# Performance work log

Measured on AMD Instinct MI355X. Metric: run time of the kernel, lower is better.

Reference implementation:

```python
import jax, jax.numpy as jnp
import numpy as np

DIM = 512
HEADS = 8
DIM_HEAD = DIM // 8          # 64
M_LAND = DIM // 2            # 256 landmarks
PINV_ITERS = 6
KS = 33                      # residual depthwise conv kernel
EPS = 1e-8
LN_EPS = 1e-5


def setup_inputs() -> dict:
    key = jax.random.key(0)
    ks = jax.random.split(key, 5)
    b, n = 2, 8192
    inner = HEADS * DIM_HEAD
    x = jax.random.normal(ks[0], (b, n, DIM), jnp.float32)
    mask = jnp.ones((b, n), jnp.bool_)
    w_qkv = jax.random.normal(ks[1], (DIM, 3 * inner), jnp.float32) / np.sqrt(DIM)
    w_out = jax.random.normal(ks[2], (inner, DIM), jnp.float32) / np.sqrt(inner)
    b_out = jnp.zeros((DIM,), jnp.float32)
    conv_w = jax.random.normal(ks[3], (HEADS, 1, KS, 1), jnp.float32) / np.sqrt(KS)
    ln_w = jnp.ones((DIM,), jnp.float32)
    ln_b = jnp.zeros((DIM,), jnp.float32)
    return dict(x=x, mask=mask, ln_w=ln_w, ln_b=ln_b,
                w_qkv=w_qkv, w_out=w_out, b_out=b_out, conv_w=conv_w)


def _moore_penrose_pinv(x, iters):
    # lucidrains iterative pinv: z0 = x^T / (max(col_sums) * max(row_sums))
    abs_x = jnp.abs(x)
    col = abs_x.sum(-1)
    row = abs_x.sum(-2)
    z = jnp.swapaxes(x, -1, -2) / (jnp.max(col) * jnp.max(row))
    I = jnp.eye(x.shape[-1], dtype=x.dtype)
    for _ in range(iters):
        xz = x @ z
        z = 0.25 * z @ (13 * I - xz @ (15 * I - xz @ (7 * I - xz)))
    return z


def reference(x, mask, ln_w, ln_b, w_qkv, w_out, b_out, conv_w):
    b, n, _ = x.shape
    # LayerNorm (pre-norm)
    mu = x.mean(-1, keepdims=True)
    var = ((x - mu) ** 2).mean(-1, keepdims=True)
    xn = (x - mu) / jnp.sqrt(var + LN_EPS) * ln_w + ln_b
    # front-pad seq to multiple of num_landmarks (static; no-op when divisible)
    pad = (M_LAND - n % M_LAND) % M_LAND
    if pad:
        xn = jnp.pad(xn, ((0, 0), (pad, 0), (0, 0)))
        mask = jnp.pad(mask, ((0, 0), (pad, 0)), constant_values=False)
    N = n + pad
    qkv = xn @ w_qkv
    q, k, v = jnp.split(qkv, 3, axis=-1)
    rs = lambda t: t.reshape(b, N, HEADS, DIM_HEAD).transpose(0, 2, 1, 3)  # b h N d
    q, k, v = rs(q), rs(k), rs(v)
    m3 = mask[:, None, :]                       # b 1 N
    mf = m3[..., None].astype(q.dtype)
    q, k, v = q * mf, k * mf, v * mf
    q = q * (DIM_HEAD ** -0.5)
    l = N // M_LAND                             # tokens per landmark
    ql = q.reshape(b, HEADS, M_LAND, l, DIM_HEAD).sum(3)
    kl = k.reshape(b, HEADS, M_LAND, l, DIM_HEAD).sum(3)
    m_land_sum = m3.astype(q.dtype).reshape(b, 1, M_LAND, l).sum(-1)   # b 1 M
    divisor = m_land_sum[..., None] + EPS
    ql = ql / divisor
    kl = kl / divisor
    m_land = m_land_sum > 0                     # b 1 M
    sim1 = jnp.einsum('bhid,bhjd->bhij', q, kl)    # b h N M
    sim2 = jnp.einsum('bhid,bhjd->bhij', ql, kl)   # b h M M
    sim3 = jnp.einsum('bhid,bhjd->bhij', ql, k)    # b h M N
    NEG = -jnp.finfo(q.dtype).max
    sim1 = jnp.where(m3[..., None] & m_land[..., None, :], sim1, NEG)
    sim2 = jnp.where(m_land[..., None] & m_land[..., None, :], sim2, NEG)
    sim3 = jnp.where(m_land[..., None] & m3[..., None, :], sim3, NEG)
    a1 = jax.nn.softmax(sim1, -1)
    a2 = jax.nn.softmax(sim2, -1)
    a3 = jax.nn.softmax(sim3, -1)
    a2_inv = _moore_penrose_pinv(a2, PINV_ITERS)
    out = (a1 @ a2_inv) @ (a3 @ v)              # b h N d
    # residual depthwise conv over sequence dim (per head)
    res = jax.lax.conv_general_dilated(
        v, conv_w, window_strides=(1, 1),
        padding=((KS // 2, KS // 2), (0, 0)),
        dimension_numbers=('NCHW', 'OIHW', 'NCHW'),
        feature_group_count=HEADS)
    out = out + res
    out = out.transpose(0, 2, 1, 3).reshape(b, N, HEADS * DIM_HEAD)
    out = out @ w_out + b_out                   # dropout is identity at eval
    out = out[:, -n:]
    return x + out
```

## Files before the change

kernel.cpp:

```cpp
#include <hip/hip_runtime.h>


typedef __attribute__((ext_vector_type(8))) short bf16x8;
typedef __attribute__((ext_vector_type(4))) float f32x4;

static __device__ __forceinline__ ushort f2bf(float f) {
  union { float f; unsigned u; } c; c.f = f;
  const unsigned r = c.u + 0x7fffu + ((c.u >> 16) & 1u);
  return (ushort)(r >> 16);
}
static __device__ __forceinline__ float bf2f(ushort u) {
  union { unsigned u; float f; } c; c.u = ((unsigned)u) << 16;
  return c.f;
}

typedef __attribute__((address_space(1))) const unsigned int guint;
typedef __attribute__((address_space(3))) unsigned int luint;
static __device__ __forceinline__ void gload_lds16(const void* g, void* l) {
  __builtin_amdgcn_global_load_lds((guint*)g, (luint*)l, 16, 0, 0);
}

__global__ __launch_bounds__(256) void ln_kernel(const float* __restrict__ x,
                                                 const float* __restrict__ w,
                                                 const float* __restrict__ b,
                                                 ushort* __restrict__ xn) {
  const int row = blockIdx.x;
  const int t = threadIdx.x;
  const float* xr = x + (long long)row * 512;
  float v0 = xr[t], v1 = xr[t + 256];
  __shared__ float red[8];
  float s = v0 + v1;
#pragma unroll
  for (int o = 32; o; o >>= 1) s += __shfl_xor(s, o);
  if ((t & 63) == 0) red[t >> 6] = s;
  __syncthreads();
  const float mu = (red[0] + red[1] + red[2] + red[3]) * (1.0f / 512.0f);
  const float d0 = v0 - mu, d1 = v1 - mu;
  float qs = d0 * d0 + d1 * d1;
#pragma unroll
  for (int o = 32; o; o >>= 1) qs += __shfl_xor(qs, o);
  if ((t & 63) == 0) red[4 + (t >> 6)] = qs;
  __syncthreads();
  const float var = (red[4] + red[5] + red[6] + red[7]) * (1.0f / 512.0f);
  const float rs = rsqrtf(var + 1e-5f);
  ushort* xo = xn + (long long)row * 512;
  xo[t] = f2bf(d0 * rs * w[t] + b[t]);
  xo[t + 256] = f2bf(d1 * rs * w[t + 256] + b[t + 256]);
}

__global__ __launch_bounds__(256) void convert_T_bf16(const float* __restrict__ in,
                                                      ushort* __restrict__ out,
                                                      int R, int Cc) {
  const long long i = (long long)blockIdx.x * 256 + threadIdx.x;
  if (i >= (long long)R * Cc) return;
  const int c = (int)(i / R), r = (int)(i % R);
  out[i] = f2bf(in[(long long)r * Cc + c]);
}

__global__ __launch_bounds__(256) void gemm_bf16(
    const ushort* __restrict__ A, const ushort* __restrict__ Bt,
    float* __restrict__ C, ushort* __restrict__ uq, ushort* __restrict__ uk,
    ushort* __restrict__ uv,
    const float* __restrict__ bias, const float* __restrict__ xres,
    int K, int mode) {
  const int tid = threadIdx.x;
  const int wave = tid >> 6, lane = tid & 63;
  const int quad = lane >> 4, l16 = lane & 15;

  const int gx = gridDim.x;
  const int nwg = gx * gridDim.y;
  const int hid = blockIdx.y * gx + blockIdx.x;
  const int wid = (hid & 7) * (nwg >> 3) + (hid >> 3);
  const int tm = (wid / gx) * 128, tn = (wid % gx) * 128;

  const int wr = (wave >> 1) * 64, wc = (wave & 1) * 64;
  __shared__ __align__(16) ushort As[128 * 32];
  __shared__ __align__(16) ushort Bs[128 * 32];

  f32x4 acc[4][4];
#pragma unroll
  for (int i = 0; i < 4; ++i)
#pragma unroll
    for (int j = 0; j < 4; ++j) acc[i][j] = (f32x4)0.f;

  const int r0 = tid >> 2;
  const int c0 = (tid & 3) * 8;
  const ushort* gA0 = A + (long long)(tm + r0) * K + c0;
  const ushort* gA1 = A + (long long)(tm + 64 + r0) * K + c0;
  const ushort* gB0 = Bt + (long long)(tn + r0) * K + c0;
  const ushort* gB1 = Bt + (long long)(tn + 64 + r0) * K + c0;
  ushort* lA0 = As + (wave * 64) * 8;
  ushort* lA1 = As + (256 + wave * 64) * 8;
  ushort* lB0 = Bs + (wave * 64) * 8;
  ushort* lB1 = Bs + (256 + wave * 64) * 8;

  for (int kb = 0; kb < K; kb += 32) {
    __syncthreads();
    gload_lds16(gA0 + kb, lA0);
    gload_lds16(gA1 + kb, lA1);
    gload_lds16(gB0 + kb, lB0);
    gload_lds16(gB1 + kb, lB1);
    __syncthreads();
    bf16x8 af[4], bfr[4];
#pragma unroll
    for (int t = 0; t < 4; ++t) {
      af[t] = *(const bf16x8*)&As[(wr + t * 16 + l16) * 32 + quad * 8];
      bfr[t] = *(const bf16x8*)&Bs[(wc + t * 16 + l16) * 32 + quad * 8];
    }
#pragma unroll
    for (int i = 0; i < 4; ++i)
#pragma unroll
      for (int j = 0; j < 4; ++j)
        acc[i][j] = __builtin_amdgcn_mfma_f32_16x16x32_bf16(af[i], bfr[j], acc[i][j], 0, 0, 0);
  }

  if (mode == 2) {
#pragma unroll
    for (int ti = 0; ti < 4; ++ti) {
#pragma unroll
      for (int r = 0; r < 4; ++r) {
        const int gr = tm + wr + ti * 16 + quad * 4 + r;
        const int bb = gr >> 13, nn = gr & 8191;
#pragma unroll
        for (int tj = 0; tj < 4; ++tj) {
          const int gc = tn + wc + tj * 16 + l16;
          const int part = gc >> 9, hh = (gc >> 6) & 7, dd = gc & 63;
          float val = acc[ti][tj][r];
          if (part == 0) val *= 0.125f;
          ushort* dst = (part == 0) ? uq : ((part == 1) ? uk : uv);
          dst[((((long long)(bb * 8 + hh)) << 13) + nn) * 64 + dd] = f2bf(val);
        }
      }
    }
  } else {
#pragma unroll
    for (int ti = 0; ti < 4; ++ti) {
#pragma unroll
      for (int r = 0; r < 4; ++r) {
        const long long gr = tm + wr + ti * 16 + quad * 4 + r;
#pragma unroll
        for (int tj = 0; tj < 4; ++tj) {
          const int gc = tn + wc + tj * 16 + l16;
          const long long idx = gr * 512 + gc;
          C[idx] = acc[ti][tj][r] + bias[gc] + xres[idx];
        }
      }
    }
  }
}

__global__ __launch_bounds__(256) void gemm_f32(
    const float* __restrict__ A, const float* __restrict__ B,
    float* __restrict__ C, int K, int lda, int ldb, int ldc,
    long long sA, long long sB, long long sC) {
  const int tid = threadIdx.x;
  const int batch = blockIdx.z;
  A += (long long)batch * sA;
  B += (long long)batch * sB;
  C += (long long)batch * sC;
  const int tm = blockIdx.y * 64;
  const int tn = blockIdx.x * 64;

  __shared__ float As[16][65];
  __shared__ float Bs[16][65];

  const int tx = tid & 15, ty = tid >> 4;
  const int ar = tid >> 2, ac = (tid & 3) * 4;
  const int br = tid >> 4, bc = (tid & 15) * 4;

  float acc[4][4];
#pragma unroll
  for (int i = 0; i < 4; ++i)
#pragma unroll
    for (int j = 0; j < 4; ++j) acc[i][j] = 0.f;

  for (int kb = 0; kb < K; kb += 16) {
    const float4 a4 = *(const float4*)(A + (long long)(tm + ar) * lda + kb + ac);
    const float4 b4 = *(const float4*)(B + (long long)(kb + br) * ldb + tn + bc);
    __syncthreads();
    As[ac + 0][ar] = a4.x; As[ac + 1][ar] = a4.y;
    As[ac + 2][ar] = a4.z; As[ac + 3][ar] = a4.w;
    Bs[br][bc + 0] = b4.x; Bs[br][bc + 1] = b4.y;
    Bs[br][bc + 2] = b4.z; Bs[br][bc + 3] = b4.w;
    __syncthreads();
#pragma unroll
    for (int kk = 0; kk < 16; ++kk) {
      float av[4], bv[4];
#pragma unroll
      for (int i = 0; i < 4; ++i) av[i] = As[kk][ty * 4 + i];
#pragma unroll
      for (int j = 0; j < 4; ++j) bv[j] = Bs[kk][tx * 4 + j];
#pragma unroll
      for (int i = 0; i < 4; ++i)
#pragma unroll
        for (int j = 0; j < 4; ++j) acc[i][j] = fmaf(av[i], bv[j], acc[i][j]);
    }
  }
#pragma unroll
  for (int i = 0; i < 4; ++i) {
    const long long r = tm + ty * 4 + i;
#pragma unroll
    for (int j = 0; j < 4; ++j) C[r * ldc + tn + tx * 4 + j] = acc[i][j];
  }
}

__global__ __launch_bounds__(256) void gemm_split(
    const ushort* __restrict__ Ah, const ushort* __restrict__ Al,
    const ushort* __restrict__ BTh, const ushort* __restrict__ BTl,
    const ushort* __restrict__ D1h, const ushort* __restrict__ D1l,
    const ushort* __restrict__ D2h, const ushort* __restrict__ D2l,
    ushort* __restrict__ Ch, ushort* __restrict__ Cl,
    ushort* __restrict__ CTh, ushort* __restrict__ CTl,
    float alpha, float beta1, float beta2,
    long long sBT, long long sC, int ldc) {
  const int tid = threadIdx.x;
  const int wave = tid >> 6, lane = tid & 63;
  const int quad = lane >> 4, l16 = lane & 15;
  const int tc = blockIdx.x * 32, tr = blockIdx.y * 64;
  const int bh = blockIdx.z;
  const bool hasAl = (Al != nullptr);
  const bool hasBl = (BTl != nullptr);
  __shared__ ushort TBh[64][36];
  __shared__ ushort TBl[64][36];

  const ushort* A_h = Ah + (long long)bh * 65536 + (long long)(tr + wave * 16 + l16) * 256;
  const ushort* A_l = (hasAl ? Al : Ah) + (long long)bh * 65536 +
                      (long long)(tr + wave * 16 + l16) * 256;
  const ushort* B_h0 = BTh + (long long)bh * sBT + (long long)(tc + l16) * 256;
  const ushort* B_l0 = (hasBl ? BTl : BTh) + (long long)bh * sBT +
                       (long long)(tc + l16) * 256;

  f32x4 acc[2];
  acc[0] = (f32x4)0.f; acc[1] = (f32x4)0.f;

#pragma unroll
  for (int kc = 0; kc < 8; ++kc) {
    const int ko = kc * 32 + quad * 8;
    const bf16x8 a_h = *(const bf16x8*)(A_h + ko);
    bf16x8 a_l;
    if (hasAl) a_l = *(const bf16x8*)(A_l + ko);
#pragma unroll
    for (int ct = 0; ct < 2; ++ct) {
      const bf16x8 b_h = *(const bf16x8*)(B_h0 + ct * 4096 + ko);
      acc[ct] = __builtin_amdgcn_mfma_f32_16x16x32_bf16(a_h, b_h, acc[ct], 0, 0, 0);
      if (hasBl) {
        const bf16x8 b_l = *(const bf16x8*)(B_l0 + ct * 4096 + ko);
        acc[ct] = __builtin_amdgcn_mfma_f32_16x16x32_bf16(a_h, b_l, acc[ct], 0, 0, 0);
      }
      if (hasAl)
        acc[ct] = __builtin_amdgcn_mfma_f32_16x16x32_bf16(a_l, b_h, acc[ct], 0, 0, 0);
    }
  }

#pragma unroll
  for (int ct = 0; ct < 2; ++ct) {
#pragma unroll
    for (int r = 0; r < 4; ++r) {
      const int rl = wave * 16 + quad * 4 + r;
      const int clc = ct * 16 + l16;
      float val = alpha * acc[ct][r];
      if (D1h) {
        const long long di = (long long)bh * 65536 + (long long)(tr + rl) * 256 + tc + clc;
        float d = bf2f(D1h[di]);
        if (D1l) d += bf2f(D1l[di]);
        val += beta1 * d;
      }
      if (D2h) {
        const long long di = (long long)bh * 65536 + (long long)(tr + rl) * 256 + tc + clc;
        float d = bf2f(D2h[di]);
        if (D2l) d += bf2f(D2l[di]);
        val += beta2 * d;
      }
      const ushort h = f2bf(val);
      TBh[rl][clc] = h;
      TBl[rl][clc] = f2bf(val - bf2f(h));
    }
  }
  __syncthreads();
  if (Ch) {
    const int rl = tid >> 2, seg = (tid & 3) * 8;
    const long long ci = (long long)bh * sC + (long long)(tr + rl) * ldc + tc + seg;
    *(uint4*)&Ch[ci] = *(const uint4*)&TBh[rl][seg];
    if (Cl) *(uint4*)&Cl[ci] = *(const uint4*)&TBl[rl][seg];
  }
  if (CTh) {
    const int clc = tid >> 3, seg = (tid & 7) * 8;
    union { uint4 u; ushort s[8]; } th, tl;
#pragma unroll
    for (int j = 0; j < 8; ++j) {
      th.s[j] = TBh[seg + j][clc];
      tl.s[j] = TBl[seg + j][clc];
    }
    const long long gi = (long long)bh * 65536 + (long long)(tc + clc) * 256 + tr + seg;
    *(uint4*)&CTh[gi] = th.u;
    if (CTl) *(uint4*)&CTl[gi] = tl.u;
  }
}

__global__ __launch_bounds__(64) void landmark_kernel(
    const ushort* __restrict__ q, const ushort* __restrict__ k,
    float* __restrict__ qlf, float* __restrict__ klTf,
    ushort* __restrict__ qlb, ushort* __restrict__ klb) {
  const int bh = blockIdx.y, i = blockIdx.x, d = threadIdx.x;
  const long long base = (((long long)bh << 13) + i * 32) * 64 + d;
  float sq = 0.f, sk = 0.f;
#pragma unroll
  for (int j = 0; j < 32; ++j) {
    sq += bf2f(q[base + j * 64]);
    sk += bf2f(k[base + j * 64]);
  }
  const float mq = sq * (1.0f / 32.0f), mk = sk * (1.0f / 32.0f);
  qlf[((long long)bh * 256 + i) * 64 + d] = mq;
  klTf[((long long)bh * 64 + d) * 256 + i] = mk;
  qlb[((long long)bh * 256 + i) * 64 + d] = f2bf(mq);
  klb[((long long)bh * 256 + i) * 64 + d] = f2bf(mk);
}

__global__ __launch_bounds__(256) void softmax256(float* __restrict__ a) {
  const long long row = (long long)blockIdx.x * 4 + (threadIdx.x >> 6);
  const int lane = threadIdx.x & 63;
  float* p = a + row * 256 + lane * 4;
  float4 vv = *(float4*)p;
  float m = fmaxf(fmaxf(vv.x, vv.y), fmaxf(vv.z, vv.w));
#pragma unroll
  for (int o = 32; o; o >>= 1) m = fmaxf(m, __shfl_xor(m, o));
  vv.x = __expf(vv.x - m); vv.y = __expf(vv.y - m);
  vv.z = __expf(vv.z - m); vv.w = __expf(vv.w - m);
  float s = vv.x + vv.y + vv.z + vv.w;
#pragma unroll
  for (int o = 32; o; o >>= 1) s += __shfl_xor(s, o);
  const float inv = 1.0f / s;
  vv.x *= inv; vv.y *= inv; vv.z *= inv; vv.w *= inv;
  *(float4*)p = vv;
}

__global__ __launch_bounds__(256) void flash_mfma(
    const ushort* __restrict__ Q, const ushort* __restrict__ K,
    const ushort* __restrict__ V, float* __restrict__ Out,
    const ushort* __restrict__ CV,
    float* __restrict__ Opart, float* __restrict__ Mpart,
    float* __restrict__ Lpart,
    long long sQ, long long sK, long long sV, long long sO,
    int iters, int nsplit) {
  const int bh = blockIdx.z, mt = blockIdx.y, ns = blockIdx.x;
  const int tid = threadIdx.x;
  const int wave = tid >> 6, lane = tid & 63;
  const int quad = lane >> 4, l16 = lane & 15;
  __shared__ ushort Vt[64][72];
  __shared__ ushort Ps[64][72];

  const ushort* Qb = Q + (long long)bh * sQ + (long long)(mt * 64) * 64;
  const ushort* Kb = K + (long long)bh * sK + (long long)(ns * iters * 64) * 64;
  const ushort* Vb = V + (long long)bh * sV + (long long)(ns * iters * 64) * 64;

  bf16x8 aq[2];
#pragma unroll
  for (int kc = 0; kc < 2; ++kc)
    aq[kc] = *(const bf16x8*)(Qb + (long long)(wave * 16 + l16) * 64 + kc * 32 + quad * 8);

  f32x4 acc[4];
  float mrow[4], lrow[4];
#pragma unroll
  for (int dt = 0; dt < 4; ++dt) acc[dt] = (f32x4)0.f;
#pragma unroll
  for (int r = 0; r < 4; ++r) { mrow[r] = -1e30f; lrow[r] = 0.f; }

  for (int it = 0; it < iters; ++it) {
    __syncthreads();
    for (int i = tid; i < 512; i += 256) {
      const int key = i & 63, c8 = (i >> 6) * 8;
      union { uint4 u; ushort s[8]; } t;
      t.u = *(const uint4*)(Vb + (long long)(it * 64 + key) * 64 + c8);
#pragma unroll
      for (int j = 0; j < 8; ++j) Vt[c8 + j][key] = t.s[j];
    }
    f32x4 sfr[4];
#pragma unroll
    for (int kt = 0; kt < 4; ++kt) {
      sfr[kt] = (f32x4)0.f;
#pragma unroll
      for (int kc = 0; kc < 2; ++kc) {
        const bf16x8 bk = *(const bf16x8*)(Kb +
            (long long)(it * 64 + kt * 16 + l16) * 64 + kc * 32 + quad * 8);
        sfr[kt] = __builtin_amdgcn_mfma_f32_16x16x32_bf16(aq[kc], bk, sfr[kt], 0, 0, 0);
      }
    }
#pragma unroll
    for (int r = 0; r < 4; ++r) {
      float rm = fmaxf(fmaxf(sfr[0][r], sfr[1][r]), fmaxf(sfr[2][r], sfr[3][r]));
#pragma unroll
      for (int off = 1; off < 16; off <<= 1) rm = fmaxf(rm, __shfl_xor(rm, off));
      const float mn = fmaxf(mrow[r], rm);
      const float scv = __expf(mrow[r] - mn);
      float rs = 0.f;
#pragma unroll
      for (int kt = 0; kt < 4; ++kt) {
        const float p = __expf(sfr[kt][r] - mn);
        sfr[kt][r] = p;
        rs += p;
      }
#pragma unroll
      for (int off = 1; off < 16; off <<= 1) rs += __shfl_xor(rs, off);
      lrow[r] = lrow[r] * scv + rs;
      mrow[r] = mn;
#pragma unroll
      for (int dt = 0; dt < 4; ++dt) acc[dt][r] *= scv;
#pragma unroll
      for (int kt = 0; kt < 4; ++kt)
        Ps[wave * 16 + quad * 4 + r][kt * 16 + l16] = f2bf(sfr[kt][r]);
    }
    __syncthreads();
#pragma unroll
    for (int kc = 0; kc < 2; ++kc) {
      const bf16x8 ap = *(const bf16x8*)&Ps[wave * 16 + l16][kc * 32 + quad * 8];
#pragma unroll
      for (int dt = 0; dt < 4; ++dt) {
        const bf16x8 bv = *(const bf16x8*)&Vt[dt * 16 + l16][kc * 32 + quad * 8];
        acc[dt] = __builtin_amdgcn_mfma_f32_16x16x32_bf16(ap, bv, acc[dt], 0, 0, 0);
      }
    }
  }

  if (nsplit == 1) {
    if (CV) {
      const int b = bh >> 3, h = bh & 7;
      const ushort* cvb = CV + (((long long)bh << 13) + mt * 64) * 64;
      ushort* Ob = (ushort*)Out + ((long long)(b * 8192 + mt * 64)) * 512 + h * 64;
#pragma unroll
      for (int r = 0; r < 4; ++r) {
        const float inv = 1.0f / lrow[r];
        const int row = wave * 16 + quad * 4 + r;
#pragma unroll
        for (int dt = 0; dt < 4; ++dt) {
          const int col = dt * 16 + l16;
          const float val = acc[dt][r] * inv + bf2f(cvb[(long long)row * 64 + col]);
          Ob[(long long)row * 512 + col] = f2bf(val);
        }
      }
    } else {
      ushort* Ob = (ushort*)Out + (long long)bh * sO + (long long)(mt * 64) * 64;
#pragma unroll
      for (int r = 0; r < 4; ++r) {
        const float inv = 1.0f / lrow[r];
        const int row = wave * 16 + quad * 4 + r;
#pragma unroll
        for (int dt = 0; dt < 4; ++dt)
          Ob[(long long)row * 64 + dt * 16 + l16] = f2bf(acc[dt][r] * inv);
      }
    }
  } else {
    const long long pbase = ((long long)(bh * gridDim.y + mt) * nsplit + ns);
    const int row0 = wave * 16 + quad * 4;
#pragma unroll
    for (int r = 0; r < 4; ++r) {
#pragma unroll
      for (int dt = 0; dt < 4; ++dt)
        Opart[(pbase * 64 + row0 + r) * 64 + dt * 16 + l16] = acc[dt][r];
      if (l16 == 0) {
        Mpart[pbase * 64 + row0 + r] = mrow[r];
        Lpart[pbase * 64 + row0 + r] = lrow[r];
      }
    }
  }
}

__global__ __launch_bounds__(256) void flash_merge(
    const float* __restrict__ Opart, const float* __restrict__ Mpart,
    const float* __restrict__ Lpart, ushort* __restrict__ a3vTh,
    ushort* __restrict__ a3vTl, int nsplit) {
  const int bm = blockIdx.x >> 4;
  const int rg = blockIdx.x & 15;
  const int bh = bm >> 2, mt = bm & 3;
  const int c = threadIdx.x & 63, rb = threadIdx.x >> 6;
  const int r = rg * 4 + rb;
  float ms = -1e30f;
  for (int ns = 0; ns < nsplit; ++ns)
    ms = fmaxf(ms, Mpart[(bm * nsplit + ns) * 64 + r]);
  float L = 0.f, O = 0.f;
  for (int ns = 0; ns < nsplit; ++ns) {
    const float w = __expf(Mpart[(bm * nsplit + ns) * 64 + r] - ms);
    L += w * Lpart[(bm * nsplit + ns) * 64 + r];
    O += w * Opart[((long long)(bm * nsplit + ns) * 64 + r) * 64 + c];
  }
  const float val = O / L;
  const ushort h = f2bf(val);
  const long long ti = (long long)bh * 16384 + (long long)c * 256 + mt * 64 + r;
  a3vTh[ti] = h;
  a3vTl[ti] = f2bf(val - bf2f(h));
}

__global__ void pm_init(float* __restrict__ pm) {
  if (threadIdx.x < 2) pm[threadIdx.x] = 0.f;
}

__global__ __launch_bounds__(256) void a2_sums(const float* __restrict__ a2,
                                               float* __restrict__ pm) {
  const int p = blockIdx.x, bh = blockIdx.y;
  const float* m = a2 + (long long)bh * 65536;
  const int tid = threadIdx.x;
  __shared__ float red[4];
  {
    const int r = p * 32 + (tid >> 3);
    const int c0 = (tid & 7) * 32;
    float s = 0.f;
#pragma unroll 8
    for (int j = 0; j < 32; ++j) s += m[r * 256 + c0 + j];
    s += __shfl_xor(s, 1); s += __shfl_xor(s, 2); s += __shfl_xor(s, 4);
    float mx = s;
#pragma unroll
    for (int o = 8; o < 64; o <<= 1) mx = fmaxf(mx, __shfl_xor(mx, o));
    if ((tid & 63) == 0) red[tid >> 6] = mx;
    __syncthreads();
    if (tid == 0) {
      mx = fmaxf(fmaxf(red[0], red[1]), fmaxf(red[2], red[3]));
      atomicMax((int*)&pm[0], __float_as_int(mx));
    }
    __syncthreads();
  }
  {
    const int c = p * 32 + (tid >> 3);
    const int r0 = (tid & 7) * 32;
    float s = 0.f;
#pragma unroll 8
    for (int j = 0; j < 32; ++j) s += m[(r0 + j) * 256 + c];
    s += __shfl_xor(s, 1); s += __shfl_xor(s, 2); s += __shfl_xor(s, 4);
    float mx = s;
#pragma unroll
    for (int o = 8; o < 64; o <<= 1) mx = fmaxf(mx, __shfl_xor(mx, o));
    if ((tid & 63) == 0) red[tid >> 6] = mx;
    __syncthreads();
    if (tid == 0) {
      mx = fmaxf(fmaxf(red[0], red[1]), fmaxf(red[2], red[3]));
      atomicMax((int*)&pm[1], __float_as_int(mx));
    }
  }
}

__global__ __launch_bounds__(256) void pinv_init(
    const float* __restrict__ a2, const float* __restrict__ pm,
    ushort* __restrict__ a2h, ushort* __restrict__ a2l,
    ushort* __restrict__ zh, ushort* __restrict__ zTh) {
  const int bh = blockIdx.y;
  const float s = 1.0f / (pm[0] * pm[1]);
  const long long base = (long long)bh * 65536;
  const int i0 = blockIdx.x * 4096;
  for (int t = threadIdx.x; t < 4096; t += 256) {
    const int idx = i0 + t;
    const float v = a2[base + idx];
    const ushort h = f2bf(v);
    a2h[base + idx] = h;
    a2l[base + idx] = f2bf(v - bf2f(h));
    zTh[base + idx] = f2bf(v * s);
    const float vt = a2[base + ((long long)(idx & 255) << 8) + (idx >> 8)] * s;
    zh[base + idx] = f2bf(vt);
  }
}

__global__ __launch_bounds__(256) void conv_store(const ushort* __restrict__ v,
                                                  const float* __restrict__ w,
                                                  ushort* __restrict__ cv) {
  const int bh = blockIdx.y;
  const int n0 = blockIdx.x * 128;
  const int h = bh & 7;
  __shared__ float vs[160][64];
  __shared__ float ws[33];
  if (threadIdx.x < 33) ws[threadIdx.x] = w[h * 33 + threadIdx.x];
  for (int i = threadIdx.x; i < 160 * 8; i += 256) {
    const int r = i >> 3, c8 = (i & 7) * 8;
    const int n = n0 - 16 + r;
    if (n >= 0 && n < 8192) {
      union { uint4 u; ushort s[8]; } t;
      t.u = *(const uint4*)(v + (((long long)bh << 13) + n) * 64 + c8);
#pragma unroll
      for (int j = 0; j < 8; ++j) vs[r][c8 + j] = bf2f(t.s[j]);
    } else {
#pragma unroll
      for (int j = 0; j < 8; ++j) vs[r][c8 + j] = 0.f;
    }
  }
  __syncthreads();
  const int d = threadIdx.x & 63, r0 = threadIdx.x >> 6;
  for (int rr = r0; rr < 128; rr += 4) {
    float acc = 0.f;
#pragma unroll
    for (int kk = 0; kk < 33; ++kk) acc += ws[kk] * vs[rr + kk][d];
    cv[(((long long)bh << 13) + n0 + rr) * 64 + d] = f2bf(acc);
  }
}

static inline void launch_split(hipStream_t st, int gridX,
    const ushort* Ah, const ushort* Al,
    const ushort* BTh, const ushort* BTl, long long sBT,
    const ushort* D1h, const ushort* D1l, float beta1,
    const ushort* D2h, const ushort* D2l, float beta2,
    ushort* Ch, ushort* Cl, ushort* CTh, ushort* CTl,
    long long sC, int ldc, float alpha) {
  dim3 grid((unsigned)gridX, 4, 16);
  hipLaunchKernelGGL(gemm_split, grid, dim3(256), 0, st, Ah, Al, BTh, BTl,
                     D1h, D1l, D2h, D2l, Ch, Cl, CTh, CTl,
                     alpha, beta1, beta2, sBT, sC, ldc);
}

extern "C" void kernel_launch(void* const* d_in, const int* in_sizes, int n_in,
                              void* d_out, int out_size, void* d_ws, size_t ws_size,
                              hipStream_t stream) {
  const float* x = (const float*)d_in[0];
  const float* ln_w = (const float*)d_in[2];
  const float* ln_b = (const float*)d_in[3];
  const float* w_qkv = (const float*)d_in[4];
  const float* w_out = (const float*)d_in[5];
  const float* b_out = (const float*)d_in[6];
  const float* conv_w = (const float*)d_in[7];
  float* out = (float*)d_out;

  float* ws = (float*)d_ws;
  float* R = ws;
  float* a2   = R + 10485760LL;
  float* qlf  = a2 + 1048576LL;
  float* klTf = qlf + 262144LL;
  float* pm   = klTf + 262144LL;
  ushort* q_bf   = (ushort*)(pm + 64);
  ushort* k_bf   = q_bf + 8388608LL;
  ushort* v_bf   = k_bf + 8388608LL;
  ushort* xn_bf  = v_bf + 8388608LL;
  ushort* ql_bf  = xn_bf + 8388608LL;
  ushort* kl_bf  = ql_bf + 262144LL;
  ushort* tb_bf  = kl_bf + 262144LL;
  ushort* wqT_bf = tb_bf + 262144LL;
  ushort* woT_bf = wqT_bf + 786432LL;
  ushort* a2h    = woT_bf + 262144LL;
  ushort* a2l    = a2h + 1048576LL;
  ushort* a3vTh  = a2l + 1048576LL;
  ushort* a3vTl  = a3vTh + 262144LL;

  float* Opart = R;
  float* Mpart = R + 4194304LL;
  float* Lpart = R + 4194304LL + 65536;
  ushort* cb = (ushort*)R;
  ushort* zah = cb;                ushort* zal = cb + 1048576LL;
  ushort* zaTh = cb + 2097152LL;   ushort* zaTl = cb + 3145728LL;
  ushort* zbh = cb + 4194304LL;    ushort* zbl = cb + 5242880LL;
  ushort* zbTh = cb + 6291456LL;   ushort* zbTl = cb + 7340032LL;
  ushort* Ph = cb + 8388608LL;     ushort* Pl = cb + 9437184LL;
  ushort* PTh = cb + 10485760LL;   ushort* PTl = cb + 11534336LL;
  ushort* P2h = cb + 12582912LL;   ushort* P2l = cb + 13631488LL;
  ushort* P2Th = cb + 14680064LL;  ushort* P2Tl = cb + 15728640LL;
  ushort* T2Th = cb + 18874368LL;  ushort* T2Tl = cb + 19922944LL;
  ushort* ao2_bf = (ushort*)R;
  ushort* cv_bf  = (ushort*)R + 8388608LL;

  hipLaunchKernelGGL(convert_T_bf16, dim3(3072), dim3(256), 0, stream,
                     w_qkv, wqT_bf, 512, 1536);
  hipLaunchKernelGGL(convert_T_bf16, dim3(1024), dim3(256), 0, stream,
                     w_out, woT_bf, 512, 512);
  hipLaunchKernelGGL(ln_kernel, dim3(16384), dim3(256), 0, stream, x, ln_w, ln_b, xn_bf);
  hipLaunchKernelGGL(gemm_bf16, dim3(12, 128), dim3(256), 0, stream,
                     xn_bf, wqT_bf, nullptr, q_bf, k_bf, v_bf, nullptr, nullptr, 512, 2);
  hipLaunchKernelGGL(landmark_kernel, dim3(256, 16), dim3(64), 0, stream,
                     q_bf, k_bf, qlf, klTf, ql_bf, kl_bf);
  {
    dim3 g(4, 4, 16);
    hipLaunchKernelGGL(gemm_f32, g, dim3(256), 0, stream, qlf, klTf, a2,
                       64, 64, 256, 256, 16384LL, 16384LL, 65536LL);
  }
  hipLaunchKernelGGL(softmax256, dim3(1024), dim3(256), 0, stream, a2);
  hipLaunchKernelGGL(flash_mfma, dim3(16, 4, 16), dim3(256), 0, stream,
                     ql_bf, k_bf, v_bf, (float*)nullptr, (const ushort*)nullptr,
                     Opart, Mpart, Lpart,
                     16384LL, 524288LL, 524288LL, 0LL, 8, 16);
  hipLaunchKernelGGL(flash_merge, dim3(1024), dim3(256), 0, stream,
                     Opart, Mpart, Lpart, a3vTh, a3vTl, 16);
  hipLaunchKernelGGL(pm_init, dim3(1), dim3(64), 0, stream, pm);
  hipLaunchKernelGGL(a2_sums, dim3(8, 16), dim3(256), 0, stream, a2, pm);
  hipLaunchKernelGGL(pinv_init, dim3(16, 16), dim3(256), 0, stream, a2, pm,
                     a2h, a2l, zah, zaTh);
  ushort *zh = zah, *zTh = zaTh;
  ushort *wh = zbh, *wTh = zbTh;
  for (int it = 0; it < 5; ++it) {
    launch_split(stream, 8, a2h, nullptr, zTh, nullptr, 65536,
                 nullptr, nullptr, 0.f, nullptr, nullptr, 0.f,
                 Ph, nullptr, PTh, nullptr, 65536, 256, 1.f);
    launch_split(stream, 8, Ph, nullptr, PTh, nullptr, 65536,
                 nullptr, nullptr, 0.f, nullptr, nullptr, 0.f,
                 P2h, nullptr, P2Th, nullptr, 65536, 256, 1.f);
    launch_split(stream, 8, Ph, nullptr, P2Th, nullptr, 65536,
                 Ph, nullptr, 15.f, P2h, nullptr, -7.f,
                 nullptr, nullptr, T2Th, nullptr, 65536, 256, 1.f);
    launch_split(stream, 8, zh, nullptr, T2Th, nullptr, 65536,
                 zh, nullptr, 3.25f, nullptr, nullptr, 0.f,
                 wh, nullptr, wTh, nullptr, 65536, 256, -0.25f);
    ushort* t;
    t = zh; zh = wh; wh = t;
    t = zTh; zTh = wTh; wTh = t;
  }
  launch_split(stream, 8, a2h, a2l, zTh, nullptr, 65536,
               nullptr, nullptr, 0.f, nullptr, nullptr, 0.f,
               Ph, Pl, PTh, PTl, 65536, 256, 1.f);
  launch_split(stream, 8, Ph, Pl, PTh, PTl, 65536,
               nullptr, nullptr, 0.f, nullptr, nullptr, 0.f,
               P2h, P2l, P2Th, P2Tl, 65536, 256, 1.f);
  launch_split(stream, 8, Ph, Pl, P2Th, P2Tl, 65536,
               Ph, Pl, 15.f, P2h, P2l, -7.f,
               nullptr, nullptr, T2Th, T2Tl, 65536, 256, 1.f);
  launch_split(stream, 8, zh, nullptr, T2Th, T2Tl, 65536,
               zh, nullptr, 3.25f, nullptr, nullptr, 0.f,
               wh, zal, nullptr, nullptr, 65536, 256, -0.25f);
  launch_split(stream, 2, wh, zal, a3vTh, a3vTl, 16384,
               nullptr, nullptr, 0.f, nullptr, nullptr, 0.f,
               tb_bf, nullptr, nullptr, nullptr, 16384, 64, 1.f);
  hipLaunchKernelGGL(conv_store, dim3(64, 16), dim3(256), 0, stream, v_bf, conv_w, cv_bf);
  hipLaunchKernelGGL(flash_mfma, dim3(1, 128, 16), dim3(256), 0, stream,
                     q_bf, kl_bf, tb_bf, (float*)ao2_bf, cv_bf,
                     (float*)nullptr, (float*)nullptr, (float*)nullptr,
                     524288LL, 16384LL, 16384LL, 0LL, 4, 1);
  hipLaunchKernelGGL(gemm_bf16, dim3(4, 128), dim3(256), 0, stream,
                     ao2_bf, woT_bf, out, nullptr, nullptr, nullptr, b_out, x, 512, 3);
}
```

Measured before the change: 624.2 us.

## Fuse Newton-Schulz pinv GEMM chain into one cooperative kernel with grid syncs

Measured after the change: 1.994 ms. +219.4%, slower.

```diff
diff --git a/kernel.cpp b/kernel.cpp
--- a/kernel.cpp
+++ b/kernel.cpp
@@ -1,4 +1,7 @@
 #include <hip/hip_runtime.h>
+#include <hip/hip_cooperative_groups.h>
+
+namespace cg = cooperative_groups;
 
 
 typedef __attribute__((ext_vector_type(8))) short bf16x8;
@@ -204,7 +207,7 @@
   }
 }
 
-__global__ __launch_bounds__(256) void gemm_split(
+static __device__ void chain_stage(
     const ushort* __restrict__ Ah, const ushort* __restrict__ Al,
     const ushort* __restrict__ BTh, const ushort* __restrict__ BTl,
     const ushort* __restrict__ D1h, const ushort* __restrict__ D1l,
@@ -212,7 +215,8 @@
     ushort* __restrict__ Ch, ushort* __restrict__ Cl,
     ushort* __restrict__ CTh, ushort* __restrict__ CTl,
     float alpha, float beta1, float beta2,
-    long long sBT, long long sC, int ldc) {
+    long long sBT, long long sC, int ldc,
+    ushort (*TBh)[36], ushort (*TBl)[36]) {
   const int tid = threadIdx.x;
   const int wave = tid >> 6, lane = tid & 63;
   const int quad = lane >> 4, l16 = lane & 15;
@@ -220,8 +224,6 @@
   const int bh = blockIdx.z;
   const bool hasAl = (Al != nullptr);
   const bool hasBl = (BTl != nullptr);
-  __shared__ ushort TBh[64][36];
-  __shared__ ushort TBl[64][36];
 
   const ushort* A_h = Ah + (long long)bh * 65536 + (long long)(tr + wave * 16 + l16) * 256;
   const ushort* A_l = (hasAl ? Al : Ah) + (long long)bh * 65536 +
@@ -295,6 +297,63 @@
     *(uint4*)&CTh[gi] = th.u;
     if (CTl) *(uint4*)&CTl[gi] = tl.u;
   }
+}
+
+__global__ __launch_bounds__(256, 2) void pinv_chain(
+    const ushort* __restrict__ a2h, const ushort* __restrict__ a2l,
+    ushort* zah, ushort* zal, ushort* zaTh,
+    ushort* zbh, ushort* zbTh,
+    ushort* Ph, ushort* Pl, ushort* PTh, ushort* PTl,
+    ushort* P2h, ushort* P2l, ushort* P2Th, ushort* P2Tl,
+    ushort* T2Th, ushort* T2Tl,
+    const ushort* __restrict__ a3vTh, const ushort* __restrict__ a3vTl,
+    ushort* tb) {
+  cg::grid_group grid = cg::this_grid();
+  __shared__ ushort TBh[64][36];
+  __shared__ ushort TBl[64][36];
+
+  for (int it = 0; it < 5; ++it) {
+    const ushort* zh = (it & 1) ? zbh : zah;
+    const ushort* zTh = (it & 1) ? zbTh : zaTh;
+    ushort* wh = (it & 1) ? zah : zbh;
+    ushort* wTh = (it & 1) ? zaTh : zbTh;
+    chain_stage(a2h, nullptr, zTh, nullptr,
+                nullptr, nullptr, 0, nullptr,
+                Ph, nullptr, PTh, nullptr, 1.f, 0.f, 0.f, 65536, 65536, 256, TBh, TBl);
+    grid.sync();
+    chain_stage(Ph, nullptr, PTh, nullptr,
+                nullptr, nullptr, nullptr, nullptr,
+                P2h, nullptr, P2Th, nullptr, 1.f, 0.f, 0.f, 65536, 65536, 256, TBh, TBl);
+    grid.sync();
+    chain_stage(Ph, nullptr, P2Th, nullptr,
+                Ph, nullptr, P2h, nullptr,
+                nullptr, nullptr, T2Th, nullptr, 1.f, 15.f, -7.f, 65536, 65536, 256, TBh, TBl);
+    grid.sync();
+    chain_stage(zh, nullptr, T2Th, nullptr,
+                zh, nullptr, nullptr, nullptr,
+                wh, nullptr, wTh, nullptr, -0.25f, 3.25f, 0.f, 65536, 65536, 256, TBh, TBl);
+    grid.sync();
+  }
+  chain_stage(a2h, a2l, zbTh, nullptr,
+              nullptr, nullptr, nullptr, nullptr,
+              Ph, Pl, PTh, PTl, 1.f, 0.f, 0.f, 65536, 65536, 256, TBh, TBl);
+  grid.sync();
+  chain_stage(Ph, Pl, PTh, PTl,
+              nullptr, nullptr, nullptr, nullptr,
+              P2h, P2l, P2Th, P2Tl, 1.f, 0.f, 0.f, 65536, 65536, 256, TBh, TBl);
+  grid.sync();
+  chain_stage(Ph, Pl, P2Th, P2Tl,
+              Ph, Pl, P2h, P2l,
+              nullptr, nullptr, T2Th, T2Tl, 1.f, 15.f, -7.f, 65536, 65536, 256, TBh, TBl);
+  grid.sync();
+  chain_stage(zbh, nullptr, T2Th, T2Tl,
+              zbh, nullptr, nullptr, nullptr,
+              zah, zal, nullptr, nullptr, -0.25f, 3.25f, 0.f, 65536, 65536, 256, TBh, TBl);
+  grid.sync();
+  if (blockIdx.x < 2)
+    chain_stage(zah, zal, a3vTh, a3vTl,
+                nullptr, nullptr, nullptr, nullptr,
+                tb, nullptr, nullptr, nullptr, 1.f, 0.f, 0.f, 16384, 16384, 64, TBh, TBl);
 }
 
 __global__ __launch_bounds__(64) void landmark_kernel(
@@ -586,19 +645,6 @@
     for (int kk = 0; kk < 33; ++kk) acc += ws[kk] * vs[rr + kk][d];
     cv[(((long long)bh << 13) + n0 + rr) * 64 + d] = f2bf(acc);
   }
-}
-
-static inline void launch_split(hipStream_t st, int gridX,
-    const ushort* Ah, const ushort* Al,
-    const ushort* BTh, const ushort* BTl, long long sBT,
-    const ushort* D1h, const ushort* D1l, float beta1,
-    const ushort* D2h, const ushort* D2l, float beta2,
-    ushort* Ch, ushort* Cl, ushort* CTh, ushort* CTl,
-    long long sC, int ldc, float alpha) {
-  dim3 grid((unsigned)gridX, 4, 16);
-  hipLaunchKernelGGL(gemm_split, grid, dim3(256), 0, st, Ah, Al, BTh, BTl,
-                     D1h, D1l, D2h, D2l, Ch, Cl, CTh, CTl,
-                     alpha, beta1, beta2, sBT, sC, ldc);
 }
 
 extern "C" void kernel_launch(void* const* d_in, const int* in_sizes, int n_in,
@@ -638,9 +684,9 @@
   float* Lpart = R + 4194304LL + 65536;
   ushort* cb = (ushort*)R;
   ushort* zah = cb;                ushort* zal = cb + 1048576LL;
-  ushort* zaTh = cb + 2097152LL;   ushort* zaTl = cb + 3145728LL;
-  ushort* zbh = cb + 4194304LL;    ushort* zbl = cb + 5242880LL;
-  ushort* zbTh = cb + 6291456LL;   ushort* zbTl = cb + 7340032LL;
+  ushort* zaTh = cb + 2097152LL;
+  ushort* zbh = cb + 4194304LL;
+  ushort* zbTh = cb + 6291456LL;
   ushort* Ph = cb + 8388608LL;     ushort* Pl = cb + 9437184LL;
   ushort* PTh = cb + 10485760LL;   ushort* PTl = cb + 11534336LL;
   ushort* P2h = cb + 12582912LL;   ushort* P2l = cb + 13631488LL;
@@ -674,40 +720,13 @@
   hipLaunchKernelGGL(a2_sums, dim3(8, 16), dim3(256), 0, stream, a2, pm);
   hipLaunchKernelGGL(pinv_init, dim3(16, 16), dim3(256), 0, stream, a2, pm,
                      a2h, a2l, zah, zaTh);
-  ushort *zh = zah, *zTh = zaTh;
-  ushort *wh = zbh, *wTh = zbTh;
-  for (int it = 0; it < 5; ++it) {
-    launch_split(stream, 8, a2h, nullptr, zTh, nullptr, 65536,
-                 nullptr, nullptr, 0.f, nullptr, nullptr, 0.f,
-                 Ph, nullptr, PTh, nullptr, 65536, 256, 1.f);
-    launch_split(stream, 8, Ph, nullptr, PTh, nullptr, 65536,
-                 nullptr, nullptr, 0.f, nullptr, nullptr, 0.f,
-                 P2h, nullptr, P2Th, nullptr, 65536, 256, 1.f);
-    launch_split(stream, 8, Ph, nullptr, P2Th, nullptr, 65536,
-                 Ph, nullptr, 15.f, P2h, nullptr, -7.f,
-                 nullptr, nullptr, T2Th, nullptr, 65536, 256, 1.f);
-    launch_split(stream, 8, zh, nullptr, T2Th, nullptr, 65536,
-                 zh, nullptr, 3.25f, nullptr, nullptr, 0.f,
-                 wh, nullptr, wTh, nullptr, 65536, 256, -0.25f);
-    ushort* t;
-    t = zh; zh = wh; wh = t;
-    t = zTh; zTh = wTh; wTh = t;
-  }
-  launch_split(stream, 8, a2h, a2l, zTh, nullptr, 65536,
-               nullptr, nullptr, 0.f, nullptr, nullptr, 0.f,
-               Ph, Pl, PTh, PTl, 65536, 256, 1.f);
-  launch_split(stream, 8, Ph, Pl, PTh, PTl, 65536,
-               nullptr, nullptr, 0.f, nullptr, nullptr, 0.f,
-               P2h, P2l, P2Th, P2Tl, 65536, 256, 1.f);
-  launch_split(stream, 8, Ph, Pl, P2Th, P2Tl, 65536,
-               Ph, Pl, 15.f, P2h, P2l, -7.f,
-               nullptr, nullptr, T2Th, T2Tl, 65536, 256, 1.f);
-  launch_split(stream, 8, zh, nullptr, T2Th, T2Tl, 65536,
-               zh, nullptr, 3.25f, nullptr, nullptr, 0.f,
-               wh, zal, nullptr, nullptr, 65536, 256, -0.25f);
-  launch_split(stream, 2, wh, zal, a3vTh, a3vTl, 16384,
-               nullptr, nullptr, 0.f, nullptr, nullptr, 0.f,
-               tb_bf, nullptr, nullptr, nullptr, 16384, 64, 1.f);
+  {
+    void* cargs[] = {&a2h, &a2l, &zah, &zal, &zaTh, &zbh, &zbTh,
+                     &Ph, &Pl, &PTh, &PTl, &P2h, &P2l, &P2Th, &P2Tl,
+                     &T2Th, &T2Tl, &a3vTh, &a3vTl, &tb_bf};
+    hipLaunchCooperativeKernel((void*)pinv_chain, dim3(8, 4, 16), dim3(256),
+                               cargs, 0, stream);
+  }
   hipLaunchKernelGGL(conv_store, dim3(64, 16), dim3(256), 0, stream, v_bf, conv_w, cv_bf);
   hipLaunchKernelGGL(flash_mfma, dim3(1, 128, 16), dim3(256), 0, stream,
                      q_bf, kl_bf, tb_bf, (float*)ao2_bf, cv_bf,
```

## Track a2·z product across pinv iterations and fuse z/Y updates into one kernel

Applied to the files above, without the earlier changes.

After: 605.9 us. 2.9% less time.

```diff
diff --git a/kernel.cpp b/kernel.cpp
--- a/kernel.cpp
+++ b/kernel.cpp
@@ -204,6 +204,97 @@
   }
 }
 
+static __device__ __forceinline__ void stage_body(
+    int tc, int tr, int bh,
+    const ushort* __restrict__ Ah, const ushort* __restrict__ Al,
+    const ushort* __restrict__ BTh, const ushort* __restrict__ BTl,
+    const ushort* __restrict__ D1h, const ushort* __restrict__ D1l,
+    const ushort* __restrict__ D2h, const ushort* __restrict__ D2l,
+    ushort* __restrict__ Ch, ushort* __restrict__ Cl,
+    ushort* __restrict__ CTh, ushort* __restrict__ CTl,
+    float alpha, float beta1, float beta2,
+    long long sBT, long long sC, int ldc,
+    ushort (*TBh)[36], ushort (*TBl)[36]) {
+  const int tid = threadIdx.x;
+  const int wave = tid >> 6, lane = tid & 63;
+  const int quad = lane >> 4, l16 = lane & 15;
+  const bool hasAl = (Al != nullptr);
+  const bool hasBl = (BTl != nullptr);
+
+  const ushort* A_h = Ah + (long long)bh * 65536 + (long long)(tr + wave * 16 + l16) * 256;
+  const ushort* A_l = (hasAl ? Al : Ah) + (long long)bh * 65536 +
+                      (long long)(tr + wave * 16 + l16) * 256;
+  const ushort* B_h0 = BTh + (long long)bh * sBT + (long long)(tc + l16) * 256;
+  const ushort* B_l0 = (hasBl ? BTl : BTh) + (long long)bh * sBT +
+                       (long long)(tc + l16) * 256;
+
+  f32x4 acc[2];
+  acc[0] = (f32x4)0.f; acc[1] = (f32x4)0.f;
+
+#pragma unroll
+  for (int kc = 0; kc < 8; ++kc) {
+    const int ko = kc * 32 + quad * 8;
+    const bf16x8 a_h = *(const bf16x8*)(A_h + ko);
+    bf16x8 a_l;
+    if (hasAl) a_l = *(const bf16x8*)(A_l + ko);
+#pragma unroll
+    for (int ct = 0; ct < 2; ++ct) {
+      const bf16x8 b_h = *(const bf16x8*)(B_h0 + ct * 4096 + ko);
+      acc[ct] = __builtin_amdgcn_mfma_f32_16x16x32_bf16(a_h, b_h, acc[ct], 0, 0, 0);
+      if (hasBl) {
+        const bf16x8 b_l = *(const bf16x8*)(B_l0 + ct * 4096 + ko);
+        acc[ct] = __builtin_amdgcn_mfma_f32_16x16x32_bf16(a_h, b_l, acc[ct], 0, 0, 0);
+      }
+      if (hasAl)
+        acc[ct] = __builtin_amdgcn_mfma_f32_16x16x32_bf16(a_l, b_h, acc[ct], 0, 0, 0);
+    }
+  }
+
+#pragma unroll
+  for (int ct = 0; ct < 2; ++ct) {
+#pragma unroll
+    for (int r = 0; r < 4; ++r) {
+      const int rl = wave * 16 + quad * 4 + r;
+      const int clc = ct * 16 + l16;
+      float val = alpha * acc[ct][r];
+      if (D1h) {
+        const long long di = (long long)bh * 65536 + (long long)(tr + rl) * 256 + tc + clc;
+        float d = bf2f(D1h[di]);
+        if (D1l) d += bf2f(D1l[di]);
+        val += beta1 * d;
+      }
+      if (D2h) {
+        const long long di = (long long)bh * 65536 + (long long)(tr + rl) * 256 + tc + clc;
+        float d = bf2f(D2h[di]);
+        if (D2l) d += bf2f(D2l[di]);
+        val += beta2 * d;
+      }
+      const ushort h = f2bf(val);
+      TBh[rl][clc] = h;
+      TBl[rl][clc] = f2bf(val - bf2f(h));
+    }
+  }
+  __syncthreads();
+  if (Ch) {
+    const int rl = tid >> 2, seg = (tid & 3) * 8;
+    const long long ci = (long long)bh * sC + (long long)(tr + rl) * ldc + tc + seg;
+    *(uint4*)&Ch[ci] = *(const uint4*)&TBh[rl][seg];
+    if (Cl) *(uint4*)&Cl[ci] = *(const uint4*)&TBl[rl][seg];
+  }
+  if (CTh) {
+    const int clc = tid >> 3, seg = (tid & 7) * 8;
+    union { uint4 u; ushort s[8]; } th, tl;
+#pragma unroll
+    for (int j = 0; j < 8; ++j) {
+      th.s[j] = TBh[seg + j][clc];
+      tl.s[j] = TBl[seg + j][clc];
+    }
+    const long long gi = (long long)bh * 65536 + (long long)(tc + clc) * 256 + tr + seg;
+    *(uint4*)&CTh[gi] = th.u;
+    if (CTl) *(uint4*)&CTl[gi] = tl.u;
+  }
+}
+
 __global__ __launch_bounds__(256) void gemm_split(
     const ushort* __restrict__ Ah, const ushort* __restrict__ Al,
     const ushort* __restrict__ BTh, const ushort* __restrict__ BTl,
@@ -213,88 +304,31 @@
     ushort* __restrict__ CTh, ushort* __restrict__ CTl,
     float alpha, float beta1, float beta2,
     long long sBT, long long sC, int ldc) {
-  const int tid = threadIdx.x;
-  const int wave = tid >> 6, lane = tid & 63;
-  const int quad = lane >> 4, l16 = lane & 15;
-  const int tc = blockIdx.x * 32, tr = blockIdx.y * 64;
-  const int bh = blockIdx.z;
-  const bool hasAl = (Al != nullptr);
-  const bool hasBl = (BTl != nullptr);
   __shared__ ushort TBh[64][36];
   __shared__ ushort TBl[64][36];
-
-  const ushort* A_h = Ah + (long long)bh * 65536 + (long long)(tr + wave * 16 + l16) * 256;
-  const ushort* A_l = (hasAl ? Al : Ah) + (long long)bh * 65536 +
-                      (long long)(tr + wave * 16 + l16) * 256;
-  const ushort* B_h0 = BTh + (long long)bh * sBT + (long long)(tc + l16) * 256;
-  const ushort* B_l0 = (hasBl ? BTl : BTh) + (long long)bh * sBT +
-                       (long long)(tc + l16) * 256;
-
-  f32x4 acc[2];
-  acc[0] = (f32x4)0.f; acc[1] = (f32x4)0.f;
-
-#pragma unroll
-  for (int kc = 0; kc < 8; ++kc) {
-    const int ko = kc * 32 + quad * 8;
-    const bf16x8 a_h = *(const bf16x8*)(A_h + ko);
-    bf16x8 a_l;
-    if (hasAl) a_l = *(const bf16x8*)(A_l + ko);
-#pragma unroll
-    for (int ct = 0; ct < 2; ++ct) {
-      const bf16x8 b_h = *(const bf16x8*)(B_h0 + ct * 4096 + ko);
-      acc[ct] = __builtin_amdgcn_mfma_f32_16x16x32_bf16(a_h, b_h, acc[ct], 0, 0, 0);
-      if (hasBl) {
-        const bf16x8 b_l = *(const bf16x8*)(B_l0 + ct * 4096 + ko);
-        acc[ct] = __builtin_amdgcn_mfma_f32_16x16x32_bf16(a_h, b_l, acc[ct], 0, 0, 0);
-      }
-      if (hasAl)
-        acc[ct] = __builtin_amdgcn_mfma_f32_16x16x32_bf16(a_l, b_h, acc[ct], 0, 0, 0);
-    }
-  }
-
-#pragma unroll
-  for (int ct = 0; ct < 2; ++ct) {
-#pragma unroll
-    for (int r = 0; r < 4; ++r) {
-      const int rl = wave * 16 + quad * 4 + r;
-      const int clc = ct * 16 + l16;
-      float val = alpha * acc[ct][r];
-      if (D1h) {
-        const long long di = (long long)bh * 65536 + (long long)(tr + rl) * 256 + tc + clc;
-        float d = bf2f(D1h[di]);
-        if (D1l) d += bf2f(D1l[di]);
-        val += beta1 * d;
-      }
-      if (D2h) {
-        const long long di = (long long)bh * 65536 + (long long)(tr + rl) * 256 + tc + clc;
-        float d = bf2f(D2h[di]);
-        if (D2l) d += bf2f(D2l[di]);
-        val += beta2 * d;
-      }
-      const ushort h = f2bf(val);
-      TBh[rl][clc] = h;
-      TBl[rl][clc] = f2bf(val - bf2f(h));
-    }
-  }
-  __syncthreads();
-  if (Ch) {
-    const int rl = tid >> 2, seg = (tid & 3) * 8;
-    const long long ci = (long long)bh * sC + (long long)(tr + rl) * ldc + tc + seg;
-    *(uint4*)&Ch[ci] = *(const uint4*)&TBh[rl][seg];
-    if (Cl) *(uint4*)&Cl[ci] = *(const uint4*)&TBl[rl][seg];
-  }
-  if (CTh) {
-    const int clc = tid >> 3, seg = (tid & 7) * 8;
-    union { uint4 u; ushort s[8]; } th, tl;
-#pragma unroll
-    for (int j = 0; j < 8; ++j) {
-      th.s[j] = TBh[seg + j][clc];
-      tl.s[j] = TBl[seg + j][clc];
-    }
-    const long long gi = (long long)bh * 65536 + (long long)(tc + clc) * 256 + tr + seg;
-    *(uint4*)&CTh[gi] = th.u;
-    if (CTl) *(uint4*)&CTl[gi] = tl.u;
-  }
+  stage_body(blockIdx.x * 32, blockIdx.y * 64, blockIdx.z,
+             Ah, Al, BTh, BTl, D1h, D1l, D2h, D2l, Ch, Cl, CTh, CTl,
+             alpha, beta1, beta2, sBT, sC, ldc, TBh, TBl);
+}
+
+__global__ __launch_bounds__(256) void gemm_dual(
+    const ushort* __restrict__ zA, const ushort* __restrict__ yA,
+    const ushort* __restrict__ BT,
+    ushort* __restrict__ zC, ushort* __restrict__ zCT,
+    ushort* __restrict__ yC, ushort* __restrict__ yCT) {
+  __shared__ ushort TBh[64][36];
+  __shared__ ushort TBl[64][36];
+  const int by = blockIdx.y;
+  if (by < 4)
+    stage_body(blockIdx.x * 32, by * 64, blockIdx.z,
+               zA, nullptr, BT, nullptr, zA, nullptr, nullptr, nullptr,
+               zC, nullptr, zCT, nullptr, -0.25f, 3.25f, 0.f,
+               65536, 65536, 256, TBh, TBl);
+  else
+    stage_body(blockIdx.x * 32, (by - 4) * 64, blockIdx.z,
+               yA, nullptr, BT, nullptr, yA, nullptr, nullptr, nullptr,
+               yC, nullptr, yCT, nullptr, -0.25f, 3.25f, 0.f,
+               65536, 65536, 256, TBh, TBl);
 }
 
 __global__ __launch_bounds__(64) void landmark_kernel(
@@ -638,14 +672,16 @@
   float* Lpart = R + 4194304LL + 65536;
   ushort* cb = (ushort*)R;
   ushort* zah = cb;                ushort* zal = cb + 1048576LL;
-  ushort* zaTh = cb + 2097152LL;   ushort* zaTl = cb + 3145728LL;
-  ushort* zbh = cb + 4194304LL;    ushort* zbl = cb + 5242880LL;
-  ushort* zbTh = cb + 6291456LL;   ushort* zbTl = cb + 7340032LL;
+  ushort* zaTh = cb + 2097152LL;
+  ushort* zbh = cb + 4194304LL;
+  ushort* zbTh = cb + 6291456LL;
   ushort* Ph = cb + 8388608LL;     ushort* Pl = cb + 9437184LL;
   ushort* PTh = cb + 10485760LL;   ushort* PTl = cb + 11534336LL;
   ushort* P2h = cb + 12582912LL;   ushort* P2l = cb + 13631488LL;
   ushort* P2Th = cb + 14680064LL;  ushort* P2Tl = cb + 15728640LL;
   ushort* T2Th = cb + 18874368LL;  ushort* T2Tl = cb + 19922944LL;
+  ushort* Yah = Pl;    ushort* YaTh = PTl;
+  ushort* Ybh = P2l;   ushort* YbTh = P2Tl;
   ushort* ao2_bf = (ushort*)R;
   ushort* cv_bf  = (ushort*)R + 8388608LL;
 
@@ -674,26 +710,33 @@
   hipLaunchKernelGGL(a2_sums, dim3(8, 16), dim3(256), 0, stream, a2, pm);
   hipLaunchKernelGGL(pinv_init, dim3(16, 16), dim3(256), 0, stream, a2, pm,
                      a2h, a2l, zah, zaTh);
-  ushort *zh = zah, *zTh = zaTh;
-  ushort *wh = zbh, *wTh = zbTh;
-  for (int it = 0; it < 5; ++it) {
-    launch_split(stream, 8, a2h, nullptr, zTh, nullptr, 65536,
-                 nullptr, nullptr, 0.f, nullptr, nullptr, 0.f,
-                 Ph, nullptr, PTh, nullptr, 65536, 256, 1.f);
-    launch_split(stream, 8, Ph, nullptr, PTh, nullptr, 65536,
-                 nullptr, nullptr, 0.f, nullptr, nullptr, 0.f,
-                 P2h, nullptr, P2Th, nullptr, 65536, 256, 1.f);
-    launch_split(stream, 8, Ph, nullptr, P2Th, nullptr, 65536,
-                 Ph, nullptr, 15.f, P2h, nullptr, -7.f,
-                 nullptr, nullptr, T2Th, nullptr, 65536, 256, 1.f);
-    launch_split(stream, 8, zh, nullptr, T2Th, nullptr, 65536,
-                 zh, nullptr, 3.25f, nullptr, nullptr, 0.f,
-                 wh, nullptr, wTh, nullptr, 65536, 256, -0.25f);
-    ushort* t;
-    t = zh; zh = wh; wh = t;
-    t = zTh; zTh = wTh; wTh = t;
-  }
-  launch_split(stream, 8, a2h, a2l, zTh, nullptr, 65536,
+  launch_split(stream, 8, a2h, nullptr, zaTh, nullptr, 65536,
+               nullptr, nullptr, 0.f, nullptr, nullptr, 0.f,
+               Yah, nullptr, YaTh, nullptr, 65536, 256, 1.f);
+  {
+    ushort *zh = zah, *zTh = zaTh, *zwh = zbh, *zwTh = zbTh;
+    ushort *Yh = Yah, *YTh = YaTh, *Ywh = Ybh, *YwTh = YbTh;
+    for (int it = 0; it < 5; ++it) {
+      launch_split(stream, 8, Yh, nullptr, YTh, nullptr, 65536,
+                   nullptr, nullptr, 0.f, nullptr, nullptr, 0.f,
+                   P2h, nullptr, P2Th, nullptr, 65536, 256, 1.f);
+      launch_split(stream, 8, Yh, nullptr, P2Th, nullptr, 65536,
+                   Yh, nullptr, 15.f, P2h, nullptr, -7.f,
+                   nullptr, nullptr, T2Th, nullptr, 65536, 256, 1.f);
+      if (it < 4) {
+        hipLaunchKernelGGL(gemm_dual, dim3(8, 8, 16), dim3(256), 0, stream,
+                           zh, Yh, T2Th, zwh, zwTh, Ywh, YwTh);
+        ushort* t;
+        t = zh; zh = zwh; zwh = t;  t = zTh; zTh = zwTh; zwTh = t;
+        t = Yh; Yh = Ywh; Ywh = t;  t = YTh; YTh = YwTh; YwTh = t;
+      } else {
+        launch_split(stream, 8, zh, nullptr, T2Th, nullptr, 65536,
+                     zh, nullptr, 3.25f, nullptr, nullptr, 0.f,
+                     zwh, nullptr, zwTh, nullptr, 65536, 256, -0.25f);
+      }
+    }
+  }
+  launch_split(stream, 8, a2h, a2l, zbTh, nullptr, 65536,
                nullptr, nullptr, 0.f, nullptr, nullptr, 0.f,
                Ph, Pl, PTh, PTl, 65536, 256, 1.f);
   launch_split(stream, 8, Ph, Pl, PTh, PTl, 65536,
@@ -702,10 +745,10 @@
   launch_split(stream, 8, Ph, Pl, P2Th, P2Tl, 65536,
                Ph, Pl, 15.f, P2h, P2l, -7.f,
                nullptr, nullptr, T2Th, T2Tl, 65536, 256, 1.f);
-  launch_split(stream, 8, zh, nullptr, T2Th, T2Tl, 65536,
-               zh, nullptr, 3.25f, nullptr, nullptr, 0.f,
-               wh, zal, nullptr, nullptr, 65536, 256, -0.25f);
-  launch_split(stream, 2, wh, zal, a3vTh, a3vTl, 16384,
+  launch_split(stream, 8, zbh, nullptr, T2Th, T2Tl, 65536,
+               zbh, nullptr, 3.25f, nullptr, nullptr, 0.f,
+               zah, zal, nullptr, nullptr, 65536, 256, -0.25f);
+  launch_split(stream, 2, zah, zal, a3vTh, a3vTl, 16384,
                nullptr, nullptr, 0.f, nullptr, nullptr, 0.f,
                tb_bf, nullptr, nullptr, nullptr, 16384, 64, 1.f);
   hipLaunchKernelGGL(conv_store, dim3(64, 16), dim3(256), 0, stream, v_bf, conv_w, cv_bf);
```
